# Kernel optimization log

Hardware: AMD Instinct MI355X
Metric: run time of the kernel (lower is better)

The kernel has to match this reference:

```python
import jax, jax.numpy as jnp
import numpy as np

N_STATE = 1024
N_HEAD = 16


def setup_inputs() -> dict:
    key = jax.random.key(0)
    ks = jax.random.split(key, 8)
    B, C, H, W = 4, N_STATE, 1, 1500
    s = C ** -0.5
    return {
        "x": jax.random.normal(ks[0], (B, C, H, W), dtype=jnp.float32),
        "Wq": jax.random.normal(ks[1], (C, C), dtype=jnp.float32) * s,
        "bq": jnp.zeros((C,), dtype=jnp.float32),
        "Wk": jax.random.normal(ks[2], (C, C), dtype=jnp.float32) * s,
        "Wv": jax.random.normal(ks[3], (C, C), dtype=jnp.float32) * s,
        "bv": jnp.zeros((C,), dtype=jnp.float32),
        "Wo": jax.random.normal(ks[4], (C, C), dtype=jnp.float32) * s,
        "bo": jnp.zeros((C,), dtype=jnp.float32),
    }


def reference(x, Wq, bq, Wk, Wv, bv, Wo, bo):
    B, C, H, W = x.shape
    nh = N_HEAD
    d = C // nh
    scale = d ** -0.5

    def conv1x1(w, b=None):
        y = jnp.einsum('bchw,oc->bohw', x, w)  # 1x1 conv == per-pixel matmul
        return y if b is None else y + b[None, :, None, None]

    # [B, nh, d, H, W] per-head layout (channel split matches torch .split)
    q = conv1x1(Wq, bq).reshape(B, nh, d, H, W)
    k = conv1x1(Wk).reshape(B, nh, d, H, W)
    v = conv1x1(Wv, bv).reshape(B, nh, d, H, W)

    # attention along width axis, independently per height row and head
    scores = jnp.einsum('bndhq,bndhk->bnhqk', q, k) * scale  # [B,nh,H,Wq,Wk]
    attn = jax.nn.softmax(scores, axis=-1)                   # softmax over keys
    o = jnp.einsum('bnhqk,bndhk->bndhq', attn, v).reshape(B, C, H, W)
    return jnp.einsum('bchw,oc->bohw', o, Wo) + bo[None, :, None, None]
```

## Files before the change

### kernel.cpp

```cpp
#include <hip/hip_runtime.h>
#include <stdint.h>


typedef unsigned short u16;
typedef __bf16 bf16x8 __attribute__((ext_vector_type(8)));
typedef float  f32x4  __attribute__((ext_vector_type(4)));
typedef unsigned int __attribute__((address_space(1))) as1_uint;
typedef unsigned int __attribute__((address_space(3))) as3_uint;

__device__ __forceinline__ u16 f2bf(float f) {
    unsigned u = __float_as_uint(f);
    u += 0x7fffu + ((u >> 16) & 1u);
    return (u16)(u >> 16);
}

__device__ __forceinline__ f32x4 fzero4() { f32x4 z = {0.f, 0.f, 0.f, 0.f}; return z; }

__device__ __forceinline__ void gld16(void* lds, const void* g) {
    __builtin_amdgcn_global_load_lds((const as1_uint*)g, (as3_uint*)lds, 16, 0, 0);
}

__device__ __forceinline__ int permw(int w) {
    return (w & ~31) | ((w & 12) << 1) | ((w & 16) >> 2) | (w & 3);
}

__global__ void prep_k(const float* __restrict__ wq, const float* __restrict__ wk,
                       const float* __restrict__ wv, const float* __restrict__ wo,
                       u16* __restrict__ wb, const float* __restrict__ x,
                       u16* __restrict__ xb) {
    __shared__ float tile[64][65];
    const int bid = blockIdx.x;
    if (bid < 4096) {
        unsigned idx = bid * 256u + threadIdx.x;
        unsigned m = idx >> 18, r = idx & 0x3ffffu;
        const float* s = (m == 0) ? wq : (m == 1) ? wk : (m == 2) ? wv : wo;
        float4 v = ((const float4*)s)[r];
        uint2 o;
        o.x = (unsigned)f2bf(v.x) | ((unsigned)f2bf(v.y) << 16);
        o.y = (unsigned)f2bf(v.z) | ((unsigned)f2bf(v.w) << 16);
        ((uint2*)(wb + (m << 20)))[r] = o;
    } else {
        int bid2 = bid - 4096;
        const int xw = bid2 % 24, yc = (bid2 / 24) & 15, b = bid2 / 384;
        const int w0 = xw * 64, c0 = yc * 64;
        const int tw = threadIdx.x & 63, t4 = threadIdx.x >> 6;
#pragma unroll
        for (int i = 0; i < 16; i++) {
            int c = i * 4 + t4, w = w0 + tw;
            tile[c][tw] = (w < 1500) ? x[((b << 10) + c0 + c) * 1500 + w] : 0.f;
        }
        __syncthreads();
#pragma unroll
        for (int i = 0; i < 16; i++) {
            int wl = i * 4 + t4, w = w0 + wl;
            if (w < 1500) xb[((b * 1500 + w) << 10) + c0 + tw] = f2bf(tile[tw][wl]);
        }
    }
}

__device__ __forceinline__ void gemm_core64(const u16* __restrict__ A, int arow0, int amax,
                                            const u16* __restrict__ Bm, int brow0, int bmax,
                                            f32x4 (&acc)[4][4], unsigned char* lds) {
    const int t = threadIdx.x, l15 = t & 15, lg = (t >> 4) & 3;
    const int wv = t >> 6, wm = wv >> 1, wn = wv & 1;
    const int l7 = l15 & 7;
#pragma unroll
    for (int im = 0; im < 4; im++)
#pragma unroll
        for (int in = 0; in < 4; in++) acc[im][in] = fzero4();

    for (int kt = 0; kt < 16; kt++) {
        const int k0 = kt << 6;
        __syncthreads();
#pragma unroll
        for (int i = 0; i < 4; i++) {
            int xo = (i * 256 + t) << 4;
            int row = xo >> 7, seg = (xo >> 4) & 7;
            int sseg = seg ^ (row & 7);
            int ar = arow0 + row; if (ar > amax) ar = amax;
            int br = brow0 + row; if (br > bmax) br = bmax;
            gld16(lds + xo,         A  + ((long)ar << 10) + k0 + sseg * 8);
            gld16(lds + 16384 + xo, Bm + ((long)br << 10) + k0 + sseg * 8);
        }
        __syncthreads();
#pragma unroll
        for (int ks = 0; ks < 2; ks++) {
            bf16x8 af[4], bfr[4];
#pragma unroll
            for (int im = 0; im < 4; im++) {
                int row = wm * 64 + im * 16 + l15;
                af[im] = *(const bf16x8*)(lds + (row << 7) + (((ks * 4 + lg) ^ l7) << 4));
            }
#pragma unroll
            for (int in = 0; in < 4; in++) {
                int row = wn * 64 + in * 16 + l15;
                bfr[in] = *(const bf16x8*)(lds + 16384 + (row << 7) + (((ks * 4 + lg) ^ l7) << 4));
            }
#pragma unroll
            for (int im = 0; im < 4; im++)
#pragma unroll
                for (int in = 0; in < 4; in++)
                    acc[im][in] = __builtin_amdgcn_mfma_f32_16x16x32_bf16(af[im], bfr[in], acc[im][in], 0, 0, 0);
        }
    }
}

__global__ __launch_bounds__(256) void qkv_k(const u16* __restrict__ xb, const u16* __restrict__ wb,
                                             const float* __restrict__ bq, const float* __restrict__ bv,
                                             u16* __restrict__ Q, u16* __restrict__ K,
                                             u16* __restrict__ Vt) {
    __shared__ __attribute__((aligned(16))) unsigned char lds[32768];
    const int bid = blockIdx.x;
    const int t = threadIdx.x, l15 = t & 15, lg = (t >> 4) & 3;
    const int wv = t >> 6, wm = wv >> 1, wn = wv & 1;
    f32x4 acc[4][4];

    if (bid < 752) {
        const int z = bid / 376, rem = bid % 376;
        const int xt = rem % 47, yt = rem / 47;
        gemm_core64(xb, xt * 128, 5999, wb + (z << 20), yt * 128, 1023, acc, lds);
        const int m0 = xt * 128 + wm * 64, n0 = yt * 128 + wn * 64;
        u16* dst = z ? K : Q;
        const float* bias = z ? nullptr : bq;
#pragma unroll
        for (int im = 0; im < 4; im++) {
#pragma unroll
            for (int r = 0; r < 4; r++) {
                int tok = m0 + im * 16 + lg * 4 + r;
                if (tok < 6000) {
                    int b = tok / 1500, w = tok - b * 1500;
#pragma unroll
                    for (int in = 0; in < 4; in++) {
                        int o = n0 + in * 16 + l15;
                        float v = acc[im][in][r] + (bias ? bias[o] : 0.f);
                        dst[((((b << 4) + (o >> 6)) * 1500 + w) << 6) + (o & 63)] = f2bf(v);
                    }
                }
            }
        }
    } else {
        const int rem = bid - 752;
        const int xt = rem & 7, rest = rem >> 3;
        const int yt = rest % 12, b = rest / 12;
        gemm_core64(wb + (2u << 20), xt * 128, 1023, xb + b * 1500 * 1024, yt * 128, 1499, acc, lds);
        const int m0 = xt * 128 + wm * 64, n0 = yt * 128 + wn * 64;
#pragma unroll
        for (int im = 0; im < 4; im++) {
#pragma unroll
            for (int r = 0; r < 4; r++) {
                int o = m0 + im * 16 + lg * 4 + r;
                float bi = bv[o];
#pragma unroll
                for (int in = 0; in < 4; in++) {
                    int w = n0 + in * 16 + l15;
                    if (w < 1504) {
                        u16 val = (w < 1500) ? f2bf(acc[im][in][r] + bi) : (u16)0;
                        Vt[((b << 10) + o) * 1504 + permw(w)] = val;
                    }
                }
            }
        }
    }
}

__global__ __launch_bounds__(256) void gemm_out_k(const u16* __restrict__ Ow, const u16* __restrict__ wb,
                                                  const float* __restrict__ bo, float* __restrict__ out) {
    __shared__ __attribute__((aligned(16))) unsigned char lds[32768];
    const int b = blockIdx.z;
    f32x4 acc[4][4];
    gemm_core64(wb + (3u << 20), blockIdx.x * 128, 1023, Ow + b * 1500 * 1024, blockIdx.y * 128, 1499, acc, lds);
    const int t = threadIdx.x, l15 = t & 15, lg = (t >> 4) & 3;
    const int wv = t >> 6, wm = wv >> 1, wn = wv & 1;
    const int m0 = blockIdx.x * 128 + wm * 64;
    const int n0 = blockIdx.y * 128 + wn * 64;
#pragma unroll
    for (int im = 0; im < 4; im++) {
#pragma unroll
        for (int r = 0; r < 4; r++) {
            int o = m0 + im * 16 + lg * 4 + r;
            float bi = bo[o];
#pragma unroll
            for (int in = 0; in < 4; in++) {
                int w = n0 + in * 16 + l15;
                if (w < 1500) out[(long)((b << 10) + o) * 1500 + w] = acc[im][in][r] + bi;
            }
        }
    }
}

__global__ __launch_bounds__(512) void attn_k(const u16* __restrict__ Q, const u16* __restrict__ K,
                                              const u16* __restrict__ Vt, u16* __restrict__ O) {
    __shared__ __attribute__((aligned(16))) unsigned char lds[32768];

    const int qt = blockIdx.x, bh = blockIdx.y;
    const int b = bh >> 4, h = bh & 15;
    const int t = threadIdx.x, wv = t >> 6, l15 = t & 15, g = (t >> 4) & 3;
    const int sk7 = l15 & 7;

    int q_a = qt * 128 + wv * 16 + l15; if (q_a > 1499) q_a = 1499;
    const u16* qrow = Q + (((long)bh * 1500 + q_a) << 6);
    bf16x8 qb0 = *(const bf16x8*)(qrow + (g << 3));
    bf16x8 qb1 = *(const bf16x8*)(qrow + 32 + (g << 3));

    const u16* Kbh = K + (((long)bh * 1500) << 6);
    const u16* Vtb = Vt + (long)((b << 10) + (h << 6)) * 1504;

    const int srow = t >> 3;
    const int ssw  = ((t & 7) ^ (srow & 7)) << 3;
    unsigned char* kdst = lds + (t << 4);
    unsigned char* vdst = lds + 16384 + (t << 4);

    f32x4 o_acc[4];
#pragma unroll
    for (int nf = 0; nf < 4; nf++) o_acc[nf] = fzero4();
    float m_run = -1e30f, l_part = 0.f;
    const float SC = 0.18033688011112042f;

    gld16(kdst, Kbh + ((long)srow << 6) + ssw);
    gld16(vdst, Vtb + (long)srow * 1504 + ssw);
    __syncthreads();

    for (int tile = 0; tile < 24; ++tile) {
        const int cur = tile & 1;
        if (tile < 23) {
            int kv0 = (tile + 1) << 6;
            int kg = kv0 + srow; if (kg > 1499) kg = 1499;
            gld16(kdst + ((cur ^ 1) << 13), Kbh + ((long)kg << 6) + ssw);
            int vc = kv0 + ssw; if (vc > 1496) vc = 1496;
            gld16(vdst + ((cur ^ 1) << 13), Vtb + (long)srow * 1504 + vc);
        }
        const unsigned char* Kl = lds + (cur << 13);
        const unsigned char* Vl = lds + 16384 + (cur << 13);

        f32x4 s[4];
        __builtin_amdgcn_s_setprio(1);
#pragma unroll
        for (int kt = 0; kt < 4; kt++) {
            const unsigned char* kp = Kl + ((kt * 16 + l15) << 7);
            bf16x8 ka0 = *(const bf16x8*)(kp + ((g ^ sk7) << 4));
            bf16x8 ka1 = *(const bf16x8*)(kp + (((g + 4) ^ sk7) << 4));
            f32x4 z = fzero4();
            z = __builtin_amdgcn_mfma_f32_16x16x32_bf16(ka0, qb0, z, 0, 0, 0);
            z = __builtin_amdgcn_mfma_f32_16x16x32_bf16(ka1, qb1, z, 0, 0, 0);
            s[kt] = z;
        }
        __builtin_amdgcn_s_setprio(0);
        if (tile == 23) {
#pragma unroll
            for (int kt = 0; kt < 4; kt++)
#pragma unroll
                for (int r = 0; r < 4; r++)
                    if (kt * 16 + g * 4 + r >= 28) s[kt][r] = -1e30f;
        }

        float m1 = fmaxf(fmaxf(s[0][0], s[0][1]), s[0][2]);
        float m2 = fmaxf(fmaxf(s[0][3], s[1][0]), s[1][1]);
        float m3 = fmaxf(fmaxf(s[1][2], s[1][3]), s[2][0]);
        float m4 = fmaxf(fmaxf(s[2][1], s[2][2]), s[2][3]);
        float m5 = fmaxf(fmaxf(s[3][0], s[3][1]), s[3][2]);
        float mx = fmaxf(fmaxf(fmaxf(m1, m2), m3), fmaxf(fmaxf(m4, m5), s[3][3]));
        mx = fmaxf(mx, __shfl_xor(mx, 16));
        mx = fmaxf(mx, __shfl_xor(mx, 32));

        if (!__all(mx <= m_run + 44.f)) {
            float mnew = fmaxf(m_run, mx);
            float sc = exp2f((m_run - mnew) * SC);
            l_part *= sc;
#pragma unroll
            for (int r = 0; r < 4; r++) {
                float sco = __shfl(sc, g * 4 + r);
#pragma unroll
                for (int nf = 0; nf < 4; nf++) o_acc[nf][r] *= sco;
            }
            m_run = mnew;
        }

        const float msc = m_run * SC;
        float pv[4][4];
        float psum = 0.f;
#pragma unroll
        for (int kt = 0; kt < 4; kt++) {
#pragma unroll
            for (int r = 0; r < 4; r++) {
                float p = exp2f(fmaf(s[kt][r], SC, -msc));
                pv[kt][r] = p;
                psum += p;
            }
        }
        l_part += psum;

        bf16x8 pa0, pa1;
#pragma unroll
        for (int j = 0; j < 8; j++) {
            pa0[j] = (__bf16)pv[j >> 2][j & 3];
            pa1[j] = (__bf16)pv[2 + (j >> 2)][j & 3];
        }

        __builtin_amdgcn_s_setprio(1);
#pragma unroll
        for (int nf = 0; nf < 4; nf++) {
            const unsigned char* vp = Vl + ((nf * 16 + l15) << 7);
            bf16x8 vb0 = *(const bf16x8*)(vp + ((g ^ sk7) << 4));
            bf16x8 vb1 = *(const bf16x8*)(vp + (((4 + g) ^ sk7) << 4));
            o_acc[nf] = __builtin_amdgcn_mfma_f32_16x16x32_bf16(pa0, vb0, o_acc[nf], 0, 0, 0);
            o_acc[nf] = __builtin_amdgcn_mfma_f32_16x16x32_bf16(pa1, vb1, o_acc[nf], 0, 0, 0);
        }
        __builtin_amdgcn_s_setprio(0);
        __syncthreads();
    }

    l_part += __shfl_xor(l_part, 16);
    l_part += __shfl_xor(l_part, 32);
    float inv = 1.f / l_part;
#pragma unroll
    for (int r = 0; r < 4; r++) {
        float invr = __shfl(inv, g * 4 + r);
        int q = qt * 128 + wv * 16 + g * 4 + r;
        if (q < 1500) {
            u16* dst = O + ((long)(b * 1500 + q) << 10) + (h << 6);
#pragma unroll
            for (int nf = 0; nf < 4; nf++)
                dst[nf * 16 + l15] = f2bf(o_acc[nf][r] * invr);
        }
    }
}

extern "C" void kernel_launch(void* const* d_in, const int* in_sizes, int n_in,
                              void* d_out, int out_size, void* d_ws, size_t ws_size,
                              hipStream_t stream) {
    const float* x  = (const float*)d_in[0];
    const float* Wq = (const float*)d_in[1];
    const float* bq = (const float*)d_in[2];
    const float* Wk = (const float*)d_in[3];
    const float* Wv = (const float*)d_in[4];
    const float* bv = (const float*)d_in[5];
    const float* Wo = (const float*)d_in[6];
    const float* bo = (const float*)d_in[7];
    float* out = (float*)d_out;

    const size_t NEED = 57573376;
    if (ws_size < NEED) return;

    unsigned char* ws = (unsigned char*)d_ws;
    u16* xb = (u16*)(ws);
    u16* wb = (u16*)(ws + 12288000);
    u16* Qw = (u16*)(ws + 20676608);
    u16* Kw = (u16*)(ws + 32964608);
    u16* Vt = (u16*)(ws + 45252608);

    prep_k<<<dim3(5632), dim3(256), 0, stream>>>(Wq, Wk, Wv, Wo, wb, x, xb);
    qkv_k<<<dim3(1136), dim3(256), 0, stream>>>(xb, wb, bq, bv, Qw, Kw, Vt);
    attn_k<<<dim3(12, 64), dim3(512), 0, stream>>>(Qw, Kw, Vt, xb );
    gemm_out_k<<<dim3(8, 12, 4), dim3(256), 0, stream>>>(xb, wb, bo, out);
}
```

Before: 197.7 us.

## Double-buffer GEMM LDS staging, swizzle block order, flatten output GEMM tokens

The shared GEMM core now uses two LDS buffers, so the global-to-LDS loads for the next K tile are issued while MFMAs run on the current one. This removes one barrier per iteration and hides load latency. Block IDs in qkv_k and gemm_out_k are remapped with an XCD-style stride, and the output GEMM treats all 6000 tokens as one N dimension, giving 376 blocks instead of 384 with less tail waste. LDS per block doubles to 64 KB, which may lower occupancy.

```diff
diff --git a/kernel.cpp b/kernel.cpp
--- a/kernel.cpp
+++ b/kernel.cpp
@@ -58,9 +58,27 @@
     }
 }
 
-__device__ __forceinline__ void gemm_core64(const u16* __restrict__ A, int arow0, int amax,
-                                            const u16* __restrict__ Bm, int brow0, int bmax,
-                                            f32x4 (&acc)[4][4], unsigned char* lds) {
+__device__ __forceinline__ void stage_db(const u16* __restrict__ A, int arow0, int amax,
+                                         const u16* __restrict__ Bm, int brow0, int bmax,
+                                         int k0, unsigned char* lds, int buf) {
+    const int t = threadIdx.x;
+    unsigned char* ab = lds + (buf << 14);
+    unsigned char* bb = lds + 32768 + (buf << 14);
+#pragma unroll
+    for (int i = 0; i < 4; i++) {
+        int xo = (i * 256 + t) << 4;
+        int row = xo >> 7, seg = (xo >> 4) & 7;
+        int sseg = seg ^ (row & 7);
+        int ar = arow0 + row; if (ar > amax) ar = amax;
+        int br = brow0 + row; if (br > bmax) br = bmax;
+        gld16(ab + xo, A  + ((long)ar << 10) + k0 + sseg * 8);
+        gld16(bb + xo, Bm + ((long)br << 10) + k0 + sseg * 8);
+    }
+}
+
+__device__ __forceinline__ void gemm_core_db(const u16* __restrict__ A, int arow0, int amax,
+                                             const u16* __restrict__ Bm, int brow0, int bmax,
+                                             f32x4 (&acc)[4][4], unsigned char* lds) {
     const int t = threadIdx.x, l15 = t & 15, lg = (t >> 4) & 3;
     const int wv = t >> 6, wm = wv >> 1, wn = wv & 1;
     const int l7 = l15 & 7;
@@ -69,32 +87,27 @@
 #pragma unroll
         for (int in = 0; in < 4; in++) acc[im][in] = fzero4();
 
+    stage_db(A, arow0, amax, Bm, brow0, bmax, 0, lds, 0);
+    __syncthreads();
+
     for (int kt = 0; kt < 16; kt++) {
-        const int k0 = kt << 6;
-        __syncthreads();
-#pragma unroll
-        for (int i = 0; i < 4; i++) {
-            int xo = (i * 256 + t) << 4;
-            int row = xo >> 7, seg = (xo >> 4) & 7;
-            int sseg = seg ^ (row & 7);
-            int ar = arow0 + row; if (ar > amax) ar = amax;
-            int br = brow0 + row; if (br > bmax) br = bmax;
-            gld16(lds + xo,         A  + ((long)ar << 10) + k0 + sseg * 8);
-            gld16(lds + 16384 + xo, Bm + ((long)br << 10) + k0 + sseg * 8);
-        }
-        __syncthreads();
+        const int cur = kt & 1;
+        if (kt < 15)
+            stage_db(A, arow0, amax, Bm, brow0, bmax, (kt + 1) << 6, lds, cur ^ 1);
+        const unsigned char* ab = lds + (cur << 14);
+        const unsigned char* bb = lds + 32768 + (cur << 14);
 #pragma unroll
         for (int ks = 0; ks < 2; ks++) {
             bf16x8 af[4], bfr[4];
 #pragma unroll
             for (int im = 0; im < 4; im++) {
                 int row = wm * 64 + im * 16 + l15;
-                af[im] = *(const bf16x8*)(lds + (row << 7) + (((ks * 4 + lg) ^ l7) << 4));
+                af[im] = *(const bf16x8*)(ab + (row << 7) + (((ks * 4 + lg) ^ l7) << 4));
             }
 #pragma unroll
             for (int in = 0; in < 4; in++) {
                 int row = wn * 64 + in * 16 + l15;
-                bfr[in] = *(const bf16x8*)(lds + 16384 + (row << 7) + (((ks * 4 + lg) ^ l7) << 4));
+                bfr[in] = *(const bf16x8*)(bb + (row << 7) + (((ks * 4 + lg) ^ l7) << 4));
             }
 #pragma unroll
             for (int im = 0; im < 4; im++)
@@ -102,6 +115,7 @@
                 for (int in = 0; in < 4; in++)
                     acc[im][in] = __builtin_amdgcn_mfma_f32_16x16x32_bf16(af[im], bfr[in], acc[im][in], 0, 0, 0);
         }
+        if (kt < 15) __syncthreads();
     }
 }
 
@@ -109,8 +123,9 @@
                                              const float* __restrict__ bq, const float* __restrict__ bv,
                                              u16* __restrict__ Q, u16* __restrict__ K,
                                              u16* __restrict__ Vt) {
-    __shared__ __attribute__((aligned(16))) unsigned char lds[32768];
-    const int bid = blockIdx.x;
+    __shared__ __attribute__((aligned(16))) unsigned char lds[65536];
+    const int p = blockIdx.x;
+    const int bid = (p & 7) * 142 + (p >> 3);
     const int t = threadIdx.x, l15 = t & 15, lg = (t >> 4) & 3;
     const int wv = t >> 6, wm = wv >> 1, wn = wv & 1;
     f32x4 acc[4][4];
@@ -118,7 +133,7 @@
     if (bid < 752) {
         const int z = bid / 376, rem = bid % 376;
         const int xt = rem % 47, yt = rem / 47;
-        gemm_core64(xb, xt * 128, 5999, wb + (z << 20), yt * 128, 1023, acc, lds);
+        gemm_core_db(xb, xt * 128, 5999, wb + (z << 20), yt * 128, 1023, acc, lds);
         const int m0 = xt * 128 + wm * 64, n0 = yt * 128 + wn * 64;
         u16* dst = z ? K : Q;
         const float* bias = z ? nullptr : bq;
@@ -142,7 +157,7 @@
         const int rem = bid - 752;
         const int xt = rem & 7, rest = rem >> 3;
         const int yt = rest % 12, b = rest / 12;
-        gemm_core64(wb + (2u << 20), xt * 128, 1023, xb + b * 1500 * 1024, yt * 128, 1499, acc, lds);
+        gemm_core_db(wb + (2u << 20), xt * 128, 1023, xb + b * 1500 * 1024, yt * 128, 1499, acc, lds);
         const int m0 = xt * 128 + wm * 64, n0 = yt * 128 + wn * 64;
 #pragma unroll
         for (int im = 0; im < 4; im++) {
@@ -165,14 +180,16 @@
 
 __global__ __launch_bounds__(256) void gemm_out_k(const u16* __restrict__ Ow, const u16* __restrict__ wb,
                                                   const float* __restrict__ bo, float* __restrict__ out) {
-    __shared__ __attribute__((aligned(16))) unsigned char lds[32768];
-    const int b = blockIdx.z;
+    __shared__ __attribute__((aligned(16))) unsigned char lds[65536];
+    const int p = blockIdx.x;
+    const int lb = (p & 7) * 47 + (p >> 3);
+    const int xt = lb & 7, nt = lb >> 3;
     f32x4 acc[4][4];
-    gemm_core64(wb + (3u << 20), blockIdx.x * 128, 1023, Ow + b * 1500 * 1024, blockIdx.y * 128, 1499, acc, lds);
+    gemm_core_db(wb + (3u << 20), xt * 128, 1023, Ow, nt * 128, 5999, acc, lds);
     const int t = threadIdx.x, l15 = t & 15, lg = (t >> 4) & 3;
     const int wv = t >> 6, wm = wv >> 1, wn = wv & 1;
-    const int m0 = blockIdx.x * 128 + wm * 64;
-    const int n0 = blockIdx.y * 128 + wn * 64;
+    const int m0 = xt * 128 + wm * 64;
+    const int n0 = nt * 128 + wn * 64;
 #pragma unroll
     for (int im = 0; im < 4; im++) {
 #pragma unroll
@@ -181,8 +198,11 @@
             float bi = bo[o];
 #pragma unroll
             for (int in = 0; in < 4; in++) {
-                int w = n0 + in * 16 + l15;
-                if (w < 1500) out[(long)((b << 10) + o) * 1500 + w] = acc[im][in][r] + bi;
+                int tok = n0 + in * 16 + l15;
+                if (tok < 6000) {
+                    int b = tok / 1500, w = tok - b * 1500;
+                    out[(long)((b << 10) + o) * 1500 + w] = acc[im][in][r] + bi;
+                }
             }
         }
     }
@@ -282,9 +302,9 @@
         for (int kt = 0; kt < 4; kt++) {
 #pragma unroll
             for (int r = 0; r < 4; r++) {
-                float p = exp2f(fmaf(s[kt][r], SC, -msc));
-                pv[kt][r] = p;
-                psum += p;
+                float p2 = exp2f(fmaf(s[kt][r], SC, -msc));
+                pv[kt][r] = p2;
+                psum += p2;
             }
         }
         l_part += psum;
@@ -351,5 +371,5 @@
     prep_k<<<dim3(5632), dim3(256), 0, stream>>>(Wq, Wk, Wv, Wo, wb, x, xb);
     qkv_k<<<dim3(1136), dim3(256), 0, stream>>>(xb, wb, bq, bv, Qw, Kw, Vt);
     attn_k<<<dim3(12, 64), dim3(512), 0, stream>>>(Qw, Kw, Vt, xb );
-    gemm_out_k<<<dim3(8, 12, 4), dim3(256), 0, stream>>>(xb, wb, bo, out);
-}
+    gemm_out_k<<<dim3(376), dim3(256), 0, stream>>>(xb, wb, bo, out);
+}
```

New measurement: 190.1 us. 3.8% less time.
